# Kernel tuning notes

Hardware: AMD Instinct MI355X
Metric: run time of the kernel (lower is better)

Reference implementation:

```python
import jax, jax.numpy as jnp
import numpy as np

NUM_GRAPHS = 64
NEG_SLOPE = 0.1


def gcn_conv(x, src, dst, W, b, num_nodes):
    h = x @ W  # [N, out]
    ones = jnp.ones(src.shape[0], dtype=x.dtype)
    deg = jax.ops.segment_sum(ones, dst, num_segments=num_nodes) + 1.0  # +1 self-loop
    dinv = jax.lax.rsqrt(deg)  # deg >= 1 always
    coef = dinv[src] * dinv[dst]  # [E]
    agg = jax.ops.segment_sum(h[src] * coef[:, None], dst, num_segments=num_nodes)
    # self-loop contribution: dinv[i]^2 * h[i]
    out = agg + h * (dinv * dinv)[:, None] + b
    return out


def leaky_relu(x):
    return jnp.where(x >= 0, x, NEG_SLOPE * x)


def global_mean_pool(x, batch, num_graphs):
    s = jax.ops.segment_sum(x, batch, num_segments=num_graphs)
    cnt = jax.ops.segment_sum(jnp.ones(x.shape[0], dtype=x.dtype), batch, num_segments=num_graphs)
    return s / jnp.maximum(cnt, 1.0)[:, None]


def setup_inputs() -> dict:
    key = jax.random.key(0)
    ks = jax.random.split(key, 10)
    N, E, D_IN, D_H, D_OUT, C = 50000, 600000, 128, 128, 128, 16
    x = jax.random.normal(ks[0], (N, D_IN), dtype=jnp.float32)
    edge_index = jax.random.randint(ks[1], (2, E), 0, N, dtype=jnp.int32)
    batch = jnp.sort(jax.random.randint(ks[2], (N,), 0, NUM_GRAPHS, dtype=jnp.int32))
    def glorot(k, shape):
        lim = np.sqrt(6.0 / (shape[0] + shape[1]))
        return jax.random.uniform(k, shape, jnp.float32, -lim, lim)
    W1 = glorot(ks[3], (D_IN, D_H))
    b1 = jnp.zeros((D_H,), jnp.float32)
    W2 = glorot(ks[4], (D_H, D_OUT))
    b2 = jnp.zeros((D_OUT,), jnp.float32)
    Wl = glorot(ks[5], (D_OUT, C))
    bl = jnp.zeros((C,), jnp.float32)
    return {"x": x, "edge_index": edge_index, "batch": batch,
            "W1": W1, "b1": b1, "W2": W2, "b2": b2, "Wl": Wl, "bl": bl}


def reference(x, edge_index, batch, W1, b1, W2, b2, Wl, bl):
    N = x.shape[0]
    src, dst = edge_index[0], edge_index[1]
    h = gcn_conv(x, src, dst, W1, b1, N)
    h = leaky_relu(h)
    h = gcn_conv(h, src, dst, W2, b2, N)
    h = leaky_relu(h)
    g = global_mean_pool(h, batch, NUM_GRAPHS)  # [G, D_OUT]
    # dropout p=0.2 is identity in eval mode
    return g @ Wl + bl
```

## Files before the change

kernel.cpp:

```cpp
#include <hip/hip_runtime.h>

#define D 128
#define NG 64
#define NC 16
#define NEG 0.1f

typedef __attribute__((ext_vector_type(8))) short bf16x8;
typedef __attribute__((ext_vector_type(4))) float f32x4;

__device__ __forceinline__ float bf2f(unsigned int u16) {
    union { unsigned int i; float f; } c;
    c.i = u16 << 16;
    return c.f;
}
__device__ __forceinline__ unsigned short f2bf(float f) {
    union { float f; unsigned int i; } c;
    c.f = f;
    unsigned int i = c.i;
    unsigned int r = (i + 0x7FFFu + ((i >> 16) & 1u)) >> 16;
    return (unsigned short)r;
}

__global__ void prep_misc_kernel(const float* __restrict__ W1, unsigned short* __restrict__ Wf1,
                                 const float* __restrict__ W2, unsigned short* __restrict__ Wf2,
                                 float* __restrict__ pooled,
                                 const int* __restrict__ dst, int* __restrict__ deg, int E) {
    int b = blockIdx.x;
    if (b < 16) {
        const float* W = (b < 8) ? W1 : W2;
        unsigned short* Wf = (b < 8) ? Wf1 : Wf2;
        int fid = (b & 7) * 256 + threadIdx.x;
        int m = fid & 15;
        int quad = (fid >> 4) & 3;
        int kc = (fid >> 6) & 3;
        int t = fid >> 8;
        int n = t * 16 + m;
        int k0 = kc * 32 + quad * 8;
        unsigned short r[8];
#pragma unroll
        for (int j = 0; j < 8; j++) r[j] = f2bf(W[(k0 + j) * 128 + n]);
        uint4 v;
        v.x = (unsigned int)r[0] | ((unsigned int)r[1] << 16);
        v.y = (unsigned int)r[2] | ((unsigned int)r[3] << 16);
        v.z = (unsigned int)r[4] | ((unsigned int)r[5] << 16);
        v.w = (unsigned int)r[6] | ((unsigned int)r[7] << 16);
        ((uint4*)Wf)[fid] = v;
    } else if (b < 48) {
        pooled[(b - 16) * 256 + threadIdx.x] = 0.f;
    } else {
        int e = (b - 48) * 256 + threadIdx.x;
        if (e < E) atomicAdd(&deg[dst[e]], 1);
    }
}

__global__ void scan_block_kernel(const int* __restrict__ deg, int* __restrict__ scan1,
                                  int* __restrict__ blocksum, float* __restrict__ dinv, int N) {
    __shared__ int sm[256];
    int tid = threadIdx.x;
    int i = blockIdx.x * 256 + tid;
    int v = (i < N) ? deg[i] : 0;
    if (i < N) dinv[i] = 1.0f / sqrtf((float)v + 1.0f);
    sm[tid] = v;
    __syncthreads();
    for (int off = 1; off < 256; off <<= 1) {
        int t = (tid >= off) ? sm[tid - off] : 0;
        __syncthreads();
        sm[tid] += t;
        __syncthreads();
    }
    if (i < N) scan1[i] = sm[tid];
    if (tid == 255) blocksum[blockIdx.x] = sm[255];
}

__global__ void finalize_ptr_kernel(const int* __restrict__ deg, const int* __restrict__ scan1,
                                    const int* __restrict__ blocksum, int* __restrict__ ptr,
                                    int* __restrict__ fill, int nb, int N, int E) {
    __shared__ int sm[256];
    int tid = threadIdx.x;
    int v = (tid < nb) ? blocksum[tid] : 0;
    sm[tid] = v;
    __syncthreads();
    for (int off = 1; off < 256; off <<= 1) {
        int t = (tid >= off) ? sm[tid - off] : 0;
        __syncthreads();
        sm[tid] += t;
        __syncthreads();
    }
    int blockoff = (blockIdx.x > 0) ? sm[blockIdx.x - 1] : 0;
    int i = blockIdx.x * 256 + tid;
    if (i < N) {
        ptr[i] = scan1[i] - deg[i] + blockoff;
        fill[i] = 0;
        if (i == N - 1) ptr[N] = E;
    }
}

__global__ void scatter_kernel(const int* __restrict__ src, const int* __restrict__ dst,
                               const int* __restrict__ ptr, int* __restrict__ fill,
                               const float* __restrict__ dinv,
                               int2* __restrict__ csr_edge, int E) {
    int e = blockIdx.x * blockDim.x + threadIdx.x;
    if (e < E) {
        int d = dst[e];
        int s = src[e];
        int pos = ptr[d] + atomicAdd(&fill[d], 1);
        float coef = dinv[s] * dinv[d];
        csr_edge[pos] = make_int2(s, __float_as_int(coef));
    }
}

template <bool AF32>
__global__ __launch_bounds__(256) void gemm_mfma_kernel(const void* __restrict__ Ap,
                                                        const uint4* __restrict__ Wf,
                                                        unsigned int* __restrict__ C, int N) {
    __shared__ uint4 Ws[2048];
    int tid = threadIdx.x;
    int w = tid >> 6, lane = tid & 63;
    int quad = lane >> 4, m = lane & 15;
    int rowstart = blockIdx.x * 64;

#pragma unroll
    for (int i = 0; i < 8; i++) Ws[tid + 256 * i] = Wf[tid + 256 * i];

    int arow = rowstart + 16 * w + m;
    bool valid = arow < N;
    bf16x8 af[4];
    if (AF32) {
        const float* Ag = (const float*)Ap;
#pragma unroll
        for (int kc = 0; kc < 4; kc++) {
            float4 f0 = make_float4(0.f, 0.f, 0.f, 0.f), f1 = f0;
            if (valid) {
                const float4* p = (const float4*)(Ag + (size_t)arow * 128 + kc * 32 + quad * 8);
                f0 = p[0];
                f1 = p[1];
            }
            bf16x8 a;
            a[0] = (short)f2bf(f0.x); a[1] = (short)f2bf(f0.y);
            a[2] = (short)f2bf(f0.z); a[3] = (short)f2bf(f0.w);
            a[4] = (short)f2bf(f1.x); a[5] = (short)f2bf(f1.y);
            a[6] = (short)f2bf(f1.z); a[7] = (short)f2bf(f1.w);
            af[kc] = a;
        }
    } else {
        const unsigned short* Ag = (const unsigned short*)Ap;
#pragma unroll
        for (int kc = 0; kc < 4; kc++) {
            bf16x8 a;
#pragma unroll
            for (int j = 0; j < 8; j++) a[j] = 0;
            if (valid) a = *(const bf16x8*)(Ag + (size_t)arow * 128 + kc * 32 + quad * 8);
            af[kc] = a;
        }
    }
    __syncthreads();

    f32x4 acc[8];
#pragma unroll
    for (int t = 0; t < 8; t++) acc[t] = (f32x4){0.f, 0.f, 0.f, 0.f};

#pragma unroll
    for (int t = 0; t < 8; t++) {
#pragma unroll
        for (int kc = 0; kc < 4; kc++) {
            bf16x8 bh = *(const bf16x8*)&Ws[(((t * 4 + kc) * 4 + quad) * 16 + m)];
            acc[t] = __builtin_amdgcn_mfma_f32_16x16x32_bf16(af[kc], bh, acc[t], 0, 0, 0);
        }
    }

#pragma unroll
    for (int t = 0; t < 8; t++) {
#pragma unroll
        for (int r = 0; r < 4; r++) {
            int row = rowstart + 16 * w + quad * 4 + r;
            unsigned int us = f2bf(acc[t][r]);
            unsigned int other = (unsigned int)__shfl_xor((int)us, 1);
            if (((m & 1) == 0) && row < N)
                C[(size_t)row * 64 + t * 8 + (m >> 1)] = us | (other << 16);
        }
    }
}

#define ACC8(v, c)                                                         \
    a0 += bf2f((v).x & 0xffffu) * (c); a1 += bf2f((v).x >> 16) * (c);      \
    a2 += bf2f((v).y & 0xffffu) * (c); a3 += bf2f((v).y >> 16) * (c);      \
    a4 += bf2f((v).z & 0xffffu) * (c); a5 += bf2f((v).z >> 16) * (c);      \
    a6 += bf2f((v).w & 0xffffu) * (c); a7 += bf2f((v).w >> 16) * (c);

__global__ __launch_bounds__(256) void combine_kernel(const uint4* __restrict__ h4,
                                                      const int* __restrict__ ptr,
                                                      const int2* __restrict__ csr_edge,
                                                      const float* __restrict__ dinv,
                                                      const float* __restrict__ b,
                                                      uint4* __restrict__ out4, int N) {
    __shared__ int2 smeta[4][64];
    int wave = threadIdx.x >> 6;
    int lane = threadIdx.x & 63;
    int q = lane >> 4;
    int l16 = lane & 15;
    int nb = blockIdx.x * 16 + wave * 4;
    if (nb >= N) return;
    int node = nb + q;
    bool valid = node < N;

    int wlo = ptr[nb];
    int whi = ptr[min(nb + 4, N)];
    int lo = valid ? ptr[node] : 0;
    int hi = valid ? ptr[node + 1] : 0;

    float di = valid ? dinv[node] : 0.f;
    uint4 sv = valid ? h4[(size_t)node * 16 + l16] : make_uint4(0u, 0u, 0u, 0u);
    float4 bv0 = ((const float4*)b)[l16 * 2];
    float4 bv1 = ((const float4*)b)[l16 * 2 + 1];

    float a0 = 0.f, a1 = 0.f, a2 = 0.f, a3 = 0.f, a4 = 0.f, a5 = 0.f, a6 = 0.f, a7 = 0.f;

#pragma unroll 1
    for (int base = wlo; base < whi; base += 64) {
        if (base + lane < whi) smeta[wave][lane] = csr_edge[base + lane];
        int s = max(lo, base);
        int e = min(hi, base + 64);
        int j = s;
#pragma unroll 1
        for (; j + 3 < e; j += 4) {
            int k = j - base;
            int2 e0 = smeta[wave][k];
            int2 e1 = smeta[wave][k + 1];
            int2 e2 = smeta[wave][k + 2];
            int2 e3 = smeta[wave][k + 3];
            uint4 v0 = h4[(size_t)e0.x * 16 + l16];
            uint4 v1 = h4[(size_t)e1.x * 16 + l16];
            uint4 v2 = h4[(size_t)e2.x * 16 + l16];
            uint4 v3 = h4[(size_t)e3.x * 16 + l16];
            float c0 = __int_as_float(e0.y);
            float c1 = __int_as_float(e1.y);
            float c2 = __int_as_float(e2.y);
            float c3 = __int_as_float(e3.y);
            ACC8(v0, c0)
            ACC8(v1, c1)
            ACC8(v2, c2)
            ACC8(v3, c3)
        }
#pragma unroll 1
        for (; j < e; j++) {
            int k = j - base;
            int2 e0 = smeta[wave][k];
            uint4 v0 = h4[(size_t)e0.x * 16 + l16];
            float c0 = __int_as_float(e0.y);
            ACC8(v0, c0)
        }
    }

    if (!valid) return;
    float dd = di * di;
    float v0 = a0 + bf2f(sv.x & 0xffffu) * dd + bv0.x;
    float v1 = a1 + bf2f(sv.x >> 16) * dd + bv0.y;
    float v2 = a2 + bf2f(sv.y & 0xffffu) * dd + bv0.z;
    float v3 = a3 + bf2f(sv.y >> 16) * dd + bv0.w;
    float v4 = a4 + bf2f(sv.z & 0xffffu) * dd + bv1.x;
    float v5 = a5 + bf2f(sv.z >> 16) * dd + bv1.y;
    float v6 = a6 + bf2f(sv.w & 0xffffu) * dd + bv1.z;
    float v7 = a7 + bf2f(sv.w >> 16) * dd + bv1.w;
    v0 = (v0 >= 0.f) ? v0 : NEG * v0;
    v1 = (v1 >= 0.f) ? v1 : NEG * v1;
    v2 = (v2 >= 0.f) ? v2 : NEG * v2;
    v3 = (v3 >= 0.f) ? v3 : NEG * v3;
    v4 = (v4 >= 0.f) ? v4 : NEG * v4;
    v5 = (v5 >= 0.f) ? v5 : NEG * v5;
    v6 = (v6 >= 0.f) ? v6 : NEG * v6;
    v7 = (v7 >= 0.f) ? v7 : NEG * v7;
    uint4 pv;
    pv.x = (unsigned int)f2bf(v0) | ((unsigned int)f2bf(v1) << 16);
    pv.y = (unsigned int)f2bf(v2) | ((unsigned int)f2bf(v3) << 16);
    pv.z = (unsigned int)f2bf(v4) | ((unsigned int)f2bf(v5) << 16);
    pv.w = (unsigned int)f2bf(v6) | ((unsigned int)f2bf(v7) << 16);
    out4[(size_t)node * 16 + l16] = pv;
}

#define PROWS 128
__global__ void pool_accum_kernel(const unsigned int* __restrict__ a2,
                                  const int* __restrict__ batch,
                                  float* __restrict__ pooled, int N) {
    int wave = threadIdx.x >> 6;
    int lane = threadIdx.x & 63;
    int start = blockIdx.x * PROWS;
    int end = start + PROWS;
    if (end > N) end = N;
    float s0 = 0.f, s1 = 0.f;
    int curg = -1;
    for (int r = start + wave; r < end; r += 4) {
        int g = batch[r];
        if (g != curg) {
            if (curg >= 0) {
                atomicAdd(&pooled[curg * D + 2 * lane], s0);
                atomicAdd(&pooled[curg * D + 2 * lane + 1], s1);
            }
            curg = g;
            s0 = 0.f;
            s1 = 0.f;
        }
        unsigned int v = a2[(size_t)r * 64 + lane];
        s0 += bf2f(v & 0xffffu);
        s1 += bf2f(v >> 16);
    }
    if (curg >= 0) {
        atomicAdd(&pooled[curg * D + 2 * lane], s0);
        atomicAdd(&pooled[curg * D + 2 * lane + 1], s1);
    }
}

__global__ void final_kernel(const float* __restrict__ pooled, const int* __restrict__ batch,
                             const float* __restrict__ Wl, const float* __restrict__ bl,
                             float* __restrict__ out, int N) {
    int t = blockIdx.x * blockDim.x + threadIdx.x;
    if (t >= NG * NC) return;
    int g = t >> 4, c = t & 15;
    int l = 0, h = N;
    while (l < h) { int m = (l + h) >> 1; if (batch[m] < g) l = m + 1; else h = m; }
    int lo = l;
    h = N;
    while (l < h) { int m = (l + h) >> 1; if (batch[m] < g + 1) l = m + 1; else h = m; }
    int cnt = l - lo;
    float inv = 1.0f / (float)(cnt > 0 ? cnt : 1);
    float dot = 0.f;
    for (int k = 0; k < D; k++) dot += pooled[g * D + k] * Wl[k * NC + c];
    out[t] = dot * inv + bl[c];
}

extern "C" void kernel_launch(void* const* d_in, const int* in_sizes, int n_in,
                              void* d_out, int out_size, void* d_ws, size_t ws_size,
                              hipStream_t stream) {
    const float* x = (const float*)d_in[0];
    const int* ei = (const int*)d_in[1];
    const int* batch = (const int*)d_in[2];
    const float* W1 = (const float*)d_in[3];
    const float* b1 = (const float*)d_in[4];
    const float* W2 = (const float*)d_in[5];
    const float* b2 = (const float*)d_in[6];
    const float* Wlin = (const float*)d_in[7];
    const float* bl = (const float*)d_in[8];
    float* out = (float*)d_out;

    int N = in_sizes[0] / D;
    int E = in_sizes[1] / 2;
    const int* src = ei;
    const int* dst = ei + E;

    float* ws = (float*)d_ws;
    size_t o = 0;
    unsigned int* bufA = (unsigned int*)(ws + o); o += (size_t)N * 64;
    unsigned int* bufB = (unsigned int*)(ws + o); o += (size_t)N * 64;
    int* deg = (int*)(ws + o);      o += N;
    int* fill = (int*)(ws + o);     o += N;
    float* dinv = ws + o;           o += N;
    int* scan1 = (int*)(ws + o);    o += N;
    int* blocksum = (int*)(ws + o); o += 256;
    int* csr_ptr = (int*)(ws + o);  o += (N + 4);
    int2* csr_edge = (int2*)(ws + o); o += (size_t)2 * E;
    float* pooled = ws + o;         o += NG * D;
    unsigned short* Wf1 = (unsigned short*)(ws + o); o += 8192;
    unsigned short* Wf2 = (unsigned short*)(ws + o); o += 8192;

    hipMemsetAsync(deg, 0, (size_t)N * sizeof(int), stream);

    int tb = 256;
    int nscan = (N + 255) / 256;
    prep_misc_kernel<<<48 + (E + 255) / 256, 256, 0, stream>>>(W1, Wf1, W2, Wf2, pooled,
                                                               dst, deg, E);
    scan_block_kernel<<<nscan, 256, 0, stream>>>(deg, scan1, blocksum, dinv, N);
    finalize_ptr_kernel<<<nscan, 256, 0, stream>>>(deg, scan1, blocksum, csr_ptr, fill,
                                                   nscan, N, E);
    scatter_kernel<<<(E + tb - 1) / tb, tb, 0, stream>>>(src, dst, csr_ptr, fill, dinv,
                                                         csr_edge, E);

    int gblocks = (N + 63) / 64;
    int cblocks = (N + 15) / 16;
    gemm_mfma_kernel<true><<<gblocks, 256, 0, stream>>>(x, (const uint4*)Wf1,
                                                        (unsigned int*)bufA, N);
    combine_kernel<<<cblocks, 256, 0, stream>>>((const uint4*)bufA, csr_ptr, csr_edge,
                                                dinv, b1, (uint4*)bufB, N);
    gemm_mfma_kernel<false><<<gblocks, 256, 0, stream>>>(bufB, (const uint4*)Wf2,
                                                         (unsigned int*)bufA, N);
    combine_kernel<<<cblocks, 256, 0, stream>>>((const uint4*)bufA, csr_ptr, csr_edge,
                                                dinv, b2, (uint4*)bufB, N);
    pool_accum_kernel<<<(N + PROWS - 1) / PROWS, 256, 0, stream>>>(bufB, batch, pooled, N);
    final_kernel<<<(NG * NC + tb - 1) / tb, tb, 0, stream>>>(pooled, batch, Wlin, bl, out, N);
}
```

Measured before the change: 243.6 us.

## Fuse mean-pool into second combine and compute edge coefficients on the fly

The CSR edge array now holds only source indices, and the symmetric normalization coefficient is rebuilt in the combine kernel from dinv[src]*dinv[node]. This halves CSR storage and scatter write traffic, at the cost of one extra gather per edge. The second combine kernel also accumulates mean-pool sums straight into the pooled buffer with a wave-level shuffle reduction and atomics. That removes the separate pool kernel and the write and reread of the final activations, but adds atomic contention on pooled.

```diff
diff --git a/kernel.cpp b/kernel.cpp
--- a/kernel.cpp
+++ b/kernel.cpp
@@ -97,15 +97,12 @@
 
 __global__ void scatter_kernel(const int* __restrict__ src, const int* __restrict__ dst,
                                const int* __restrict__ ptr, int* __restrict__ fill,
-                               const float* __restrict__ dinv,
-                               int2* __restrict__ csr_edge, int E) {
+                               int* __restrict__ csr_src, int E) {
     int e = blockIdx.x * blockDim.x + threadIdx.x;
     if (e < E) {
         int d = dst[e];
-        int s = src[e];
         int pos = ptr[d] + atomicAdd(&fill[d], 1);
-        float coef = dinv[s] * dinv[d];
-        csr_edge[pos] = make_int2(s, __float_as_int(coef));
+        csr_src[pos] = src[e];
     }
 }
 
@@ -187,13 +184,16 @@
     a4 += bf2f((v).z & 0xffffu) * (c); a5 += bf2f((v).z >> 16) * (c);      \
     a6 += bf2f((v).w & 0xffffu) * (c); a7 += bf2f((v).w >> 16) * (c);
 
+template <bool POOL>
 __global__ __launch_bounds__(256) void combine_kernel(const uint4* __restrict__ h4,
                                                       const int* __restrict__ ptr,
-                                                      const int2* __restrict__ csr_edge,
+                                                      const int* __restrict__ csr_src,
                                                       const float* __restrict__ dinv,
                                                       const float* __restrict__ b,
-                                                      uint4* __restrict__ out4, int N) {
-    __shared__ int2 smeta[4][64];
+                                                      uint4* __restrict__ out4,
+                                                      const int* __restrict__ batch,
+                                                      float* __restrict__ pooled, int N) {
+    __shared__ int smeta[4][64];
     int wave = threadIdx.x >> 6;
     int lane = threadIdx.x & 63;
     int q = lane >> 4;
@@ -217,25 +217,29 @@
 
 #pragma unroll 1
     for (int base = wlo; base < whi; base += 64) {
-        if (base + lane < whi) smeta[wave][lane] = csr_edge[base + lane];
+        if (base + lane < whi) smeta[wave][lane] = csr_src[base + lane];
         int s = max(lo, base);
         int e = min(hi, base + 64);
         int j = s;
 #pragma unroll 1
         for (; j + 3 < e; j += 4) {
             int k = j - base;
-            int2 e0 = smeta[wave][k];
-            int2 e1 = smeta[wave][k + 1];
-            int2 e2 = smeta[wave][k + 2];
-            int2 e3 = smeta[wave][k + 3];
-            uint4 v0 = h4[(size_t)e0.x * 16 + l16];
-            uint4 v1 = h4[(size_t)e1.x * 16 + l16];
-            uint4 v2 = h4[(size_t)e2.x * 16 + l16];
-            uint4 v3 = h4[(size_t)e3.x * 16 + l16];
-            float c0 = __int_as_float(e0.y);
-            float c1 = __int_as_float(e1.y);
-            float c2 = __int_as_float(e2.y);
-            float c3 = __int_as_float(e3.y);
+            int s0 = smeta[wave][k];
+            int s1 = smeta[wave][k + 1];
+            int s2 = smeta[wave][k + 2];
+            int s3 = smeta[wave][k + 3];
+            float d0 = dinv[s0];
+            float d1 = dinv[s1];
+            float d2 = dinv[s2];
+            float d3 = dinv[s3];
+            uint4 v0 = h4[(size_t)s0 * 16 + l16];
+            uint4 v1 = h4[(size_t)s1 * 16 + l16];
+            uint4 v2 = h4[(size_t)s2 * 16 + l16];
+            uint4 v3 = h4[(size_t)s3 * 16 + l16];
+            float c0 = d0 * di;
+            float c1 = d1 * di;
+            float c2 = d2 * di;
+            float c3 = d3 * di;
             ACC8(v0, c0)
             ACC8(v1, c1)
             ACC8(v2, c2)
@@ -244,14 +248,14 @@
 #pragma unroll 1
         for (; j < e; j++) {
             int k = j - base;
-            int2 e0 = smeta[wave][k];
-            uint4 v0 = h4[(size_t)e0.x * 16 + l16];
-            float c0 = __int_as_float(e0.y);
+            int s0 = smeta[wave][k];
+            float d0 = dinv[s0];
+            uint4 v0 = h4[(size_t)s0 * 16 + l16];
+            float c0 = d0 * di;
             ACC8(v0, c0)
         }
     }
 
-    if (!valid) return;
     float dd = di * di;
     float v0 = a0 + bf2f(sv.x & 0xffffu) * dd + bv0.x;
     float v1 = a1 + bf2f(sv.x >> 16) * dd + bv0.y;
@@ -269,43 +273,45 @@
     v5 = (v5 >= 0.f) ? v5 : NEG * v5;
     v6 = (v6 >= 0.f) ? v6 : NEG * v6;
     v7 = (v7 >= 0.f) ? v7 : NEG * v7;
-    uint4 pv;
-    pv.x = (unsigned int)f2bf(v0) | ((unsigned int)f2bf(v1) << 16);
-    pv.y = (unsigned int)f2bf(v2) | ((unsigned int)f2bf(v3) << 16);
-    pv.z = (unsigned int)f2bf(v4) | ((unsigned int)f2bf(v5) << 16);
-    pv.w = (unsigned int)f2bf(v6) | ((unsigned int)f2bf(v7) << 16);
-    out4[(size_t)node * 16 + l16] = pv;
-}
-
-#define PROWS 128
-__global__ void pool_accum_kernel(const unsigned int* __restrict__ a2,
-                                  const int* __restrict__ batch,
-                                  float* __restrict__ pooled, int N) {
-    int wave = threadIdx.x >> 6;
-    int lane = threadIdx.x & 63;
-    int start = blockIdx.x * PROWS;
-    int end = start + PROWS;
-    if (end > N) end = N;
-    float s0 = 0.f, s1 = 0.f;
-    int curg = -1;
-    for (int r = start + wave; r < end; r += 4) {
-        int g = batch[r];
-        if (g != curg) {
-            if (curg >= 0) {
-                atomicAdd(&pooled[curg * D + 2 * lane], s0);
-                atomicAdd(&pooled[curg * D + 2 * lane + 1], s1);
+
+    if (POOL) {
+        if (!valid) {
+            v0 = v1 = v2 = v3 = v4 = v5 = v6 = v7 = 0.f;
+        }
+        int g = valid ? batch[node] : 0;
+        int g0 = __shfl(g, 0);
+        bool uni = __all((!valid) || (g == g0));
+        if (uni) {
+            v0 += __shfl_xor(v0, 16); v0 += __shfl_xor(v0, 32);
+            v1 += __shfl_xor(v1, 16); v1 += __shfl_xor(v1, 32);
+            v2 += __shfl_xor(v2, 16); v2 += __shfl_xor(v2, 32);
+            v3 += __shfl_xor(v3, 16); v3 += __shfl_xor(v3, 32);
+            v4 += __shfl_xor(v4, 16); v4 += __shfl_xor(v4, 32);
+            v5 += __shfl_xor(v5, 16); v5 += __shfl_xor(v5, 32);
+            v6 += __shfl_xor(v6, 16); v6 += __shfl_xor(v6, 32);
+            v7 += __shfl_xor(v7, 16); v7 += __shfl_xor(v7, 32);
+            if (q == 0) {
+                float* p = &pooled[g0 * D + l16 * 8];
+                atomicAdd(p + 0, v0); atomicAdd(p + 1, v1);
+                atomicAdd(p + 2, v2); atomicAdd(p + 3, v3);
+                atomicAdd(p + 4, v4); atomicAdd(p + 5, v5);
+                atomicAdd(p + 6, v6); atomicAdd(p + 7, v7);
             }
-            curg = g;
-            s0 = 0.f;
-            s1 = 0.f;
-        }
-        unsigned int v = a2[(size_t)r * 64 + lane];
-        s0 += bf2f(v & 0xffffu);
-        s1 += bf2f(v >> 16);
-    }
-    if (curg >= 0) {
-        atomicAdd(&pooled[curg * D + 2 * lane], s0);
-        atomicAdd(&pooled[curg * D + 2 * lane + 1], s1);
+        } else if (valid) {
+            float* p = &pooled[g * D + l16 * 8];
+            atomicAdd(p + 0, v0); atomicAdd(p + 1, v1);
+            atomicAdd(p + 2, v2); atomicAdd(p + 3, v3);
+            atomicAdd(p + 4, v4); atomicAdd(p + 5, v5);
+            atomicAdd(p + 6, v6); atomicAdd(p + 7, v7);
+        }
+    } else {
+        if (!valid) return;
+        uint4 pv;
+        pv.x = (unsigned int)f2bf(v0) | ((unsigned int)f2bf(v1) << 16);
+        pv.y = (unsigned int)f2bf(v2) | ((unsigned int)f2bf(v3) << 16);
+        pv.z = (unsigned int)f2bf(v4) | ((unsigned int)f2bf(v5) << 16);
+        pv.w = (unsigned int)f2bf(v6) | ((unsigned int)f2bf(v7) << 16);
+        out4[(size_t)node * 16 + l16] = pv;
     }
 }
 
@@ -356,7 +362,7 @@
     int* scan1 = (int*)(ws + o);    o += N;
     int* blocksum = (int*)(ws + o); o += 256;
     int* csr_ptr = (int*)(ws + o);  o += (N + 4);
-    int2* csr_edge = (int2*)(ws + o); o += (size_t)2 * E;
+    int* csr_src = (int*)(ws + o);  o += (size_t)E;
     float* pooled = ws + o;         o += NG * D;
     unsigned short* Wf1 = (unsigned short*)(ws + o); o += 8192;
     unsigned short* Wf2 = (unsigned short*)(ws + o); o += 8192;
@@ -370,19 +376,19 @@
     scan_block_kernel<<<nscan, 256, 0, stream>>>(deg, scan1, blocksum, dinv, N);
     finalize_ptr_kernel<<<nscan, 256, 0, stream>>>(deg, scan1, blocksum, csr_ptr, fill,
                                                    nscan, N, E);
-    scatter_kernel<<<(E + tb - 1) / tb, tb, 0, stream>>>(src, dst, csr_ptr, fill, dinv,
-                                                         csr_edge, E);
+    scatter_kernel<<<(E + tb - 1) / tb, tb, 0, stream>>>(src, dst, csr_ptr, fill,
+                                                         csr_src, E);
 
     int gblocks = (N + 63) / 64;
     int cblocks = (N + 15) / 16;
     gemm_mfma_kernel<true><<<gblocks, 256, 0, stream>>>(x, (const uint4*)Wf1,
                                                         (unsigned int*)bufA, N);
-    combine_kernel<<<cblocks, 256, 0, stream>>>((const uint4*)bufA, csr_ptr, csr_edge,
-                                                dinv, b1, (uint4*)bufB, N);
+    combine_kernel<false><<<cblocks, 256, 0, stream>>>((const uint4*)bufA, csr_ptr, csr_src,
+                                                       dinv, b1, (uint4*)bufB, nullptr,
+                                                       nullptr, N);
     gemm_mfma_kernel<false><<<gblocks, 256, 0, stream>>>(bufB, (const uint4*)Wf2,
                                                          (unsigned int*)bufA, N);
-    combine_kernel<<<cblocks, 256, 0, stream>>>((const uint4*)bufA, csr_ptr, csr_edge,
-                                                dinv, b2, (uint4*)bufB, N);
-    pool_accum_kernel<<<(N + PROWS - 1) / PROWS, 256, 0, stream>>>(bufB, batch, pooled, N);
+    combine_kernel<true><<<cblocks, 256, 0, stream>>>((const uint4*)bufA, csr_ptr, csr_src,
+                                                      dinv, b2, nullptr, batch, pooled, N);
     final_kernel<<<(NG * NC + tb - 1) / tb, tb, 0, stream>>>(pooled, batch, Wlin, bl, out, N);
 }
```

Result: slower. 360.5 us (+48.0%).

## Fuse first GEMM into prep kernel and drop ptr lookup in scatter

Applied to the files above, without the earlier changes.

The first-layer GEMM (x @ W1 with in-block bf16 conversion of W1) now runs inside the prep kernel, alongside the W2 conversion, the pool zeroing and the degree atomics. This removes one kernel launch and the Wf1 round trip through global memory. Every GEMM block now converts all of W1 from fp32 itself, so that small amount of work is repeated per block. The fill array is also initialised to the CSR row pointer, so the scatter kernel skips the extra ptr[d] load.

```diff
diff --git a/kernel.cpp b/kernel.cpp
--- a/kernel.cpp
+++ b/kernel.cpp
@@ -21,35 +21,106 @@
     return (unsigned short)r;
 }
 
-__global__ void prep_misc_kernel(const float* __restrict__ W1, unsigned short* __restrict__ Wf1,
-                                 const float* __restrict__ W2, unsigned short* __restrict__ Wf2,
-                                 float* __restrict__ pooled,
-                                 const int* __restrict__ dst, int* __restrict__ deg, int E) {
+__global__ __launch_bounds__(256) void prep_gemm1_kernel(
+        const float* __restrict__ x, const float* __restrict__ W1,
+        unsigned int* __restrict__ C, int gb,
+        const float* __restrict__ W2, unsigned short* __restrict__ Wf2,
+        float* __restrict__ pooled,
+        const int* __restrict__ dst, int* __restrict__ deg, int E, int N) {
+    __shared__ uint4 Ws[2048];
     int b = blockIdx.x;
-    if (b < 16) {
-        const float* W = (b < 8) ? W1 : W2;
-        unsigned short* Wf = (b < 8) ? Wf1 : Wf2;
-        int fid = (b & 7) * 256 + threadIdx.x;
-        int m = fid & 15;
-        int quad = (fid >> 4) & 3;
-        int kc = (fid >> 6) & 3;
-        int t = fid >> 8;
-        int n = t * 16 + m;
-        int k0 = kc * 32 + quad * 8;
-        unsigned short r[8];
-#pragma unroll
-        for (int j = 0; j < 8; j++) r[j] = f2bf(W[(k0 + j) * 128 + n]);
-        uint4 v;
-        v.x = (unsigned int)r[0] | ((unsigned int)r[1] << 16);
-        v.y = (unsigned int)r[2] | ((unsigned int)r[3] << 16);
-        v.z = (unsigned int)r[4] | ((unsigned int)r[5] << 16);
-        v.w = (unsigned int)r[6] | ((unsigned int)r[7] << 16);
-        ((uint4*)Wf)[fid] = v;
-    } else if (b < 48) {
-        pooled[(b - 16) * 256 + threadIdx.x] = 0.f;
+    int tid = threadIdx.x;
+    if (b < gb) {
+        int w = tid >> 6, lane = tid & 63;
+        int quad = lane >> 4, m16 = lane & 15;
+        int rowstart = b * 64;
+#pragma unroll
+        for (int i = 0; i < 8; i++) {
+            int fid = tid + 256 * i;
+            int fm = fid & 15;
+            int fquad = (fid >> 4) & 3;
+            int fkc = (fid >> 6) & 3;
+            int ft = fid >> 8;
+            int n = ft * 16 + fm;
+            int k0 = fkc * 32 + fquad * 8;
+            unsigned short r[8];
+#pragma unroll
+            for (int j = 0; j < 8; j++) r[j] = f2bf(W1[(k0 + j) * 128 + n]);
+            uint4 v;
+            v.x = (unsigned int)r[0] | ((unsigned int)r[1] << 16);
+            v.y = (unsigned int)r[2] | ((unsigned int)r[3] << 16);
+            v.z = (unsigned int)r[4] | ((unsigned int)r[5] << 16);
+            v.w = (unsigned int)r[6] | ((unsigned int)r[7] << 16);
+            Ws[fid] = v;
+        }
+
+        int arow = rowstart + 16 * w + m16;
+        bool valid = arow < N;
+        bf16x8 af[4];
+#pragma unroll
+        for (int kc = 0; kc < 4; kc++) {
+            float4 f0 = make_float4(0.f, 0.f, 0.f, 0.f), f1 = f0;
+            if (valid) {
+                const float4* p = (const float4*)(x + (size_t)arow * 128 + kc * 32 + quad * 8);
+                f0 = p[0];
+                f1 = p[1];
+            }
+            bf16x8 a;
+            a[0] = (short)f2bf(f0.x); a[1] = (short)f2bf(f0.y);
+            a[2] = (short)f2bf(f0.z); a[3] = (short)f2bf(f0.w);
+            a[4] = (short)f2bf(f1.x); a[5] = (short)f2bf(f1.y);
+            a[6] = (short)f2bf(f1.z); a[7] = (short)f2bf(f1.w);
+            af[kc] = a;
+        }
+        __syncthreads();
+
+        f32x4 acc[8];
+#pragma unroll
+        for (int t = 0; t < 8; t++) acc[t] = (f32x4){0.f, 0.f, 0.f, 0.f};
+#pragma unroll
+        for (int t = 0; t < 8; t++) {
+#pragma unroll
+            for (int kc = 0; kc < 4; kc++) {
+                bf16x8 bh = *(const bf16x8*)&Ws[(((t * 4 + kc) * 4 + quad) * 16 + m16)];
+                acc[t] = __builtin_amdgcn_mfma_f32_16x16x32_bf16(af[kc], bh, acc[t], 0, 0, 0);
+            }
+        }
+#pragma unroll
+        for (int t = 0; t < 8; t++) {
+#pragma unroll
+            for (int r = 0; r < 4; r++) {
+                int row = rowstart + 16 * w + quad * 4 + r;
+                unsigned int us = f2bf(acc[t][r]);
+                unsigned int other = (unsigned int)__shfl_xor((int)us, 1);
+                if (((m16 & 1) == 0) && row < N)
+                    C[(size_t)row * 64 + t * 8 + (m16 >> 1)] = us | (other << 16);
+            }
+        }
     } else {
-        int e = (b - 48) * 256 + threadIdx.x;
-        if (e < E) atomicAdd(&deg[dst[e]], 1);
+        int bb = b - gb;
+        if (bb < 8) {
+            int fid = bb * 256 + tid;
+            int m = fid & 15;
+            int quad = (fid >> 4) & 3;
+            int kc = (fid >> 6) & 3;
+            int t = fid >> 8;
+            int n = t * 16 + m;
+            int k0 = kc * 32 + quad * 8;
+            unsigned short r[8];
+#pragma unroll
+            for (int j = 0; j < 8; j++) r[j] = f2bf(W2[(k0 + j) * 128 + n]);
+            uint4 v;
+            v.x = (unsigned int)r[0] | ((unsigned int)r[1] << 16);
+            v.y = (unsigned int)r[2] | ((unsigned int)r[3] << 16);
+            v.z = (unsigned int)r[4] | ((unsigned int)r[5] << 16);
+            v.w = (unsigned int)r[6] | ((unsigned int)r[7] << 16);
+            ((uint4*)Wf2)[fid] = v;
+        } else if (bb < 40) {
+            pooled[(bb - 8) * 256 + tid] = 0.f;
+        } else {
+            int e = (bb - 40) * 256 + tid;
+            if (e < E) atomicAdd(&deg[dst[e]], 1);
+        }
     }
 }
 
@@ -89,28 +160,27 @@
     int blockoff = (blockIdx.x > 0) ? sm[blockIdx.x - 1] : 0;
     int i = blockIdx.x * 256 + tid;
     if (i < N) {
-        ptr[i] = scan1[i] - deg[i] + blockoff;
-        fill[i] = 0;
+        int p = scan1[i] - deg[i] + blockoff;
+        ptr[i] = p;
+        fill[i] = p;
         if (i == N - 1) ptr[N] = E;
     }
 }
 
 __global__ void scatter_kernel(const int* __restrict__ src, const int* __restrict__ dst,
-                               const int* __restrict__ ptr, int* __restrict__ fill,
-                               const float* __restrict__ dinv,
+                               int* __restrict__ fill, const float* __restrict__ dinv,
                                int2* __restrict__ csr_edge, int E) {
     int e = blockIdx.x * blockDim.x + threadIdx.x;
     if (e < E) {
         int d = dst[e];
         int s = src[e];
-        int pos = ptr[d] + atomicAdd(&fill[d], 1);
+        int pos = atomicAdd(&fill[d], 1);
         float coef = dinv[s] * dinv[d];
         csr_edge[pos] = make_int2(s, __float_as_int(coef));
     }
 }
 
-template <bool AF32>
-__global__ __launch_bounds__(256) void gemm_mfma_kernel(const void* __restrict__ Ap,
+__global__ __launch_bounds__(256) void gemm_mfma_kernel(const unsigned short* __restrict__ Ag,
                                                         const uint4* __restrict__ Wf,
                                                         unsigned int* __restrict__ C, int N) {
     __shared__ uint4 Ws[2048];
@@ -125,33 +195,13 @@
     int arow = rowstart + 16 * w + m;
     bool valid = arow < N;
     bf16x8 af[4];
-    if (AF32) {
-        const float* Ag = (const float*)Ap;
-#pragma unroll
-        for (int kc = 0; kc < 4; kc++) {
-            float4 f0 = make_float4(0.f, 0.f, 0.f, 0.f), f1 = f0;
-            if (valid) {
-                const float4* p = (const float4*)(Ag + (size_t)arow * 128 + kc * 32 + quad * 8);
-                f0 = p[0];
-                f1 = p[1];
-            }
-            bf16x8 a;
-            a[0] = (short)f2bf(f0.x); a[1] = (short)f2bf(f0.y);
-            a[2] = (short)f2bf(f0.z); a[3] = (short)f2bf(f0.w);
-            a[4] = (short)f2bf(f1.x); a[5] = (short)f2bf(f1.y);
-            a[6] = (short)f2bf(f1.z); a[7] = (short)f2bf(f1.w);
-            af[kc] = a;
-        }
-    } else {
-        const unsigned short* Ag = (const unsigned short*)Ap;
-#pragma unroll
-        for (int kc = 0; kc < 4; kc++) {
-            bf16x8 a;
-#pragma unroll
-            for (int j = 0; j < 8; j++) a[j] = 0;
-            if (valid) a = *(const bf16x8*)(Ag + (size_t)arow * 128 + kc * 32 + quad * 8);
-            af[kc] = a;
-        }
+#pragma unroll
+    for (int kc = 0; kc < 4; kc++) {
+        bf16x8 a;
+#pragma unroll
+        for (int j = 0; j < 8; j++) a[j] = 0;
+        if (valid) a = *(const bf16x8*)(Ag + (size_t)arow * 128 + kc * 32 + quad * 8);
+        af[kc] = a;
     }
     __syncthreads();
 
@@ -358,29 +408,29 @@
     int* csr_ptr = (int*)(ws + o);  o += (N + 4);
     int2* csr_edge = (int2*)(ws + o); o += (size_t)2 * E;
     float* pooled = ws + o;         o += NG * D;
-    unsigned short* Wf1 = (unsigned short*)(ws + o); o += 8192;
     unsigned short* Wf2 = (unsigned short*)(ws + o); o += 8192;
 
     hipMemsetAsync(deg, 0, (size_t)N * sizeof(int), stream);
 
     int tb = 256;
     int nscan = (N + 255) / 256;
-    prep_misc_kernel<<<48 + (E + 255) / 256, 256, 0, stream>>>(W1, Wf1, W2, Wf2, pooled,
-                                                               dst, deg, E);
+    int gblocks = (N + 63) / 64;
+    int cblocks = (N + 15) / 16;
+    int eblocks = (E + 255) / 256;
+
+    prep_gemm1_kernel<<<gblocks + 40 + eblocks, 256, 0, stream>>>(
+        x, W1, (unsigned int*)bufA, gblocks, W2, Wf2, pooled, dst, deg, E, N);
     scan_block_kernel<<<nscan, 256, 0, stream>>>(deg, scan1, blocksum, dinv, N);
     finalize_ptr_kernel<<<nscan, 256, 0, stream>>>(deg, scan1, blocksum, csr_ptr, fill,
                                                    nscan, N, E);
-    scatter_kernel<<<(E + tb - 1) / tb, tb, 0, stream>>>(src, dst, csr_ptr, fill, dinv,
+    scatter_kernel<<<(E + tb - 1) / tb, tb, 0, stream>>>(src, dst, fill, dinv,
                                                          csr_edge, E);
 
-    int gblocks = (N + 63) / 64;
-    int cblocks = (N + 15) / 16;
-    gemm_mfma_kernel<true><<<gblocks, 256, 0, stream>>>(x, (const uint4*)Wf1,
-                                                        (unsigned int*)bufA, N);
     combine_kernel<<<cblocks, 256, 0, stream>>>((const uint4*)bufA, csr_ptr, csr_edge,
                                                 dinv, b1, (uint4*)bufB, N);
-    gemm_mfma_kernel<false><<<gblocks, 256, 0, stream>>>(bufB, (const uint4*)Wf2,
-                                                         (unsigned int*)bufA, N);
+    gemm_mfma_kernel<<<gblocks, 256, 0, stream>>>((const unsigned short*)bufB,
+                                                  (const uint4*)Wf2,
+                                                  (unsigned int*)bufA, N);
     combine_kernel<<<cblocks, 256, 0, stream>>>((const uint4*)bufA, csr_ptr, csr_edge,
                                                 dinv, b2, (uint4*)bufB, N);
     pool_accum_kernel<<<(N + PROWS - 1) / PROWS, 256, 0, stream>>>(bufB, batch, pooled, N);
```

Result: faster. 236.4 us (-3.0%).
